# Performance work log

Hardware: AMD Instinct MI355X
Metric: run time of the kernel (lower is better)

Reference implementation:

```python
import jax, jax.numpy as jnp
import numpy as np

N_NODES = 100000
N_EDGES = 3200000


def setup_inputs() -> dict:
    key = jax.random.key(0)
    ks = jax.random.split(key, 20)
    x = jax.random.normal(ks[0], (N_NODES, 3), dtype=jnp.float32)
    edge_index = jax.random.randint(ks[1], (2, N_EDGES), 0, N_NODES, dtype=jnp.int64)

    def w(k, shape, fan_in):
        return jax.random.normal(k, shape, dtype=jnp.float32) * (1.0 / np.sqrt(fan_in))

    return {
        "x": x, "edge_index": edge_index,
        # layer 1: in=3, out=16, heads=2
        "W1": w(ks[2], (3, 32), 3), "a_src1": w(ks[3], (2, 16), 16), "a_dst1": w(ks[4], (2, 16), 16), "b1": jnp.zeros((32,), jnp.float32),
        # layer 2: in=32, out=16, heads=2
        "W2": w(ks[5], (32, 32), 32), "a_src2": w(ks[6], (2, 16), 16), "a_dst2": w(ks[7], (2, 16), 16), "b2": jnp.zeros((32,), jnp.float32),
        # layer 3: in=32, out=16, heads=1
        "W3": w(ks[8], (32, 16), 32), "a_src3": w(ks[9], (1, 16), 16), "a_dst3": w(ks[10], (1, 16), 16), "b3": jnp.zeros((16,), jnp.float32),
        # output linear 16 -> 1
        "Wout": w(ks[11], (16, 1), 16), "bout": jnp.zeros((1,), jnp.float32),
    }


def gat_layer(x, src, dst, W, a_src, a_dst, b, heads, ch, n):
    # h: [N, H, C]
    h = (x @ W).reshape(n, heads, ch)
    alpha_src = jnp.sum(h * a_src[None], axis=-1)  # [N, H]
    alpha_dst = jnp.sum(h * a_dst[None], axis=-1)  # [N, H]
    e = jax.nn.leaky_relu(alpha_src[src] + alpha_dst[dst], 0.2)  # [E, H]
    # segment softmax over incoming edges of each dst node
    m = jax.ops.segment_max(e, dst, num_segments=n)
    m = jnp.where(jnp.isfinite(m), m, 0.0)
    ex = jnp.exp(e - jax.lax.stop_gradient(m)[dst])
    s = jax.ops.segment_sum(ex, dst, num_segments=n)
    alpha = ex / (s[dst] + 1e-16)  # [E, H]
    out = jax.ops.segment_sum(h[src] * alpha[:, :, None], dst, num_segments=n)  # [N, H, C]
    return out.reshape(n, heads * ch) + b


def reference(x, edge_index, W1, a_src1, a_dst1, b1, W2, a_src2, a_dst2, b2,
              W3, a_src3, a_dst3, b3, Wout, bout):
    n = x.shape[0]
    loops = jnp.arange(n, dtype=edge_index.dtype)
    src = jnp.concatenate([edge_index[0], loops])  # PyG add_self_loops=True
    dst = jnp.concatenate([edge_index[1], loops])
    h = jax.nn.elu(gat_layer(x, src, dst, W1, a_src1, a_dst1, b1, 2, 16, n))
    h = jax.nn.elu(gat_layer(h, src, dst, W2, a_src2, a_dst2, b2, 2, 16, n))
    h = jax.nn.elu(gat_layer(h, src, dst, W3, a_src3, a_dst3, b3, 1, 16, n))
    embeddings = h
    out = jax.nn.sigmoid(h @ Wout + bout)
    return out, embeddings
```

## Files before the change

kernel.cpp:

```cpp
#include <hip/hip_runtime.h>
#include <math.h>

#define TPB 256
#define PMAX 128
#define PSH 10
#define PW  1024
#define CHUNK 8192

__device__ __forceinline__ float leaky02(float x) { return x > 0.f ? x : 0.2f * x; }
__device__ __forceinline__ float eluf(float x) { return x > 0.f ? x : (expf(x) - 1.f); }


__global__ void zero_kernel(int* __restrict__ p, int n) {
  int i = blockIdx.x * blockDim.x + threadIdx.x;
  if (i < n) p[i] = 0;
}

__global__ __launch_bounds__(256) void count_kernel(const int* __restrict__ dst, int E, int n,
                                                    int* __restrict__ counts,
                                                    int* __restrict__ pcount) {
  __shared__ int lcnt[PMAX];
  int Etot = E + n;
  int c0 = blockIdx.x * CHUNK;
  if (c0 >= Etot) return;
  int c1 = min(c0 + CHUNK, Etot);
  for (int j = threadIdx.x; j < PMAX; j += TPB) lcnt[j] = 0;
  __syncthreads();
  for (int idx = c0 + threadIdx.x; idx < c1; idx += TPB) {
    int dd = (idx < E) ? dst[idx] : (idx - E);
    atomicAdd(&lcnt[dd >> PSH], 1);
  }
  __syncthreads();
  for (int j = threadIdx.x; j < PMAX; j += TPB) {
    int v = lcnt[j];
    counts[blockIdx.x * PMAX + j] = v;
    if (v) atomicAdd(&pcount[j], v);
  }
}

__global__ void pscan_kernel(const int* __restrict__ pcount, int* __restrict__ pbase,
                             int* __restrict__ pcursor, int NP) {
  if (threadIdx.x == 0) {
    int acc = 0;
    for (int q = 0; q < NP; q++) {
      pbase[q] = acc; pcursor[q] = acc; acc += pcount[q];
    }
    pbase[NP] = acc;
  }
}

__global__ __launch_bounds__(256) void scatter_kernel(const int* __restrict__ src,
                                                      const int* __restrict__ dst,
                                                      int E, int n,
                                                      const int* __restrict__ counts,
                                                      int* __restrict__ pcursor,
                                                      unsigned* __restrict__ pstage) {
  __shared__ int lbase[PMAX];
  __shared__ int lcnt[PMAX];
  int Etot = E + n;
  int c0 = blockIdx.x * CHUNK;
  if (c0 >= Etot) return;
  int c1 = min(c0 + CHUNK, Etot);
  for (int j = threadIdx.x; j < PMAX; j += TPB) {
    int c = counts[blockIdx.x * PMAX + j];
    lbase[j] = atomicAdd(&pcursor[j], c);
    lcnt[j] = 0;
  }
  __syncthreads();
  for (int idx = c0 + threadIdx.x; idx < c1; idx += TPB) {
    int ss, dd;
    if (idx < E) { ss = src[idx]; dd = dst[idx]; }
    else         { ss = dd = idx - E; }
    int p = dd >> PSH;
    int pos = lbase[p] + atomicAdd(&lcnt[p], 1);
    pstage[pos] = ((unsigned)ss << PSH) | (unsigned)(dd & (PW - 1));
  }
}

__global__ __launch_bounds__(1024) void build_csr_kernel(const unsigned* __restrict__ pstage,
                                                         const int* __restrict__ pbase,
                                                         int nvtx,
                                                         int* __restrict__ rowptr,
                                                         int* __restrict__ csr_src) {
  __shared__ int lhist[PW];
  __shared__ int lcur[PW];
  int t = threadIdx.x;
  int p = blockIdx.x;
  int base = pbase[p];
  int end = pbase[p + 1];
  int nodebase = p << PSH;
  lhist[t] = 0;
  __syncthreads();
  for (int i = base + t; i < end; i += 1024)
    atomicAdd(&lhist[pstage[i] & (PW - 1)], 1);
  __syncthreads();
  int v = lhist[t];
  lcur[t] = v;
  __syncthreads();
  for (int off = 1; off < 1024; off <<= 1) {
    int a = (t >= off) ? lcur[t - off] : 0;
    __syncthreads();
    lcur[t] += a;
    __syncthreads();
  }
  int acc = base + lcur[t] - v;
  __syncthreads();
  lcur[t] = acc;
  int node = nodebase + t;
  if (node < nvtx) rowptr[node] = acc;
  __syncthreads();
  for (int i = base + t; i < end; i += 1024) {
    unsigned w = pstage[i];
    int pos = atomicAdd(&lcur[w & (PW - 1)], 1);
    csr_src[pos] = (int)(w >> PSH);
  }
  if (p == (int)gridDim.x - 1 && t == 0) rowptr[nvtx] = end;
}


template<int IN, int OUT, int H>
__global__ void transform_kernel(const float* __restrict__ x, const float* __restrict__ W,
                                 const float* __restrict__ a_src, const float* __restrict__ a_dst,
                                 float* __restrict__ h, float* __restrict__ asrc,
                                 float* __restrict__ adst, int n) {
  __shared__ float sW[IN * OUT];
  __shared__ float sa[2 * OUT];
  for (int i = threadIdx.x; i < IN * OUT; i += blockDim.x) sW[i] = W[i];
  if (threadIdx.x < OUT) {
    sa[threadIdx.x] = a_src[threadIdx.x];
    sa[OUT + threadIdx.x] = a_dst[threadIdx.x];
  }
  __syncthreads();
  int i = blockIdx.x * blockDim.x + threadIdx.x;
  if (i >= n) return;
  float xv[IN];
#pragma unroll
  for (int k = 0; k < IN; k++) xv[k] = x[(size_t)i * IN + k];
  float hv[OUT];
#pragma unroll
  for (int j = 0; j < OUT; j++) {
    float acc = 0.f;
#pragma unroll
    for (int k = 0; k < IN; k++) acc += xv[k] * sW[k * OUT + j];
    hv[j] = acc;
    h[(size_t)i * OUT + j] = acc;
  }
#pragma unroll
  for (int hh = 0; hh < H; hh++) {
    float as = 0.f, ad = 0.f;
#pragma unroll
    for (int c = 0; c < 16; c++) {
      as += hv[hh * 16 + c] * sa[hh * 16 + c];
      ad += hv[hh * 16 + c] * sa[OUT + hh * 16 + c];
    }
    asrc[i * H + hh] = as;
    adst[i * H + hh] = ad;
  }
}


__global__ __launch_bounds__(256) void node_gat12(
    const int* __restrict__ rowptr,
    const int* __restrict__ csr_src,
    const float* __restrict__ asrc,
    const float* __restrict__ adst,
    const float* __restrict__ hfeat,
    const float* __restrict__ bias,
    float* __restrict__ outb,
    int n) {
  __shared__ float2 s_h0[4][64];
  __shared__ float2 s_h1[4][64];
  int wid = threadIdx.x >> 6;
  int lane = threadIdx.x & 63;
  int i = (blockIdx.x * blockDim.x + threadIdx.x) >> 6;
  if (i >= n) return;
  int start = rowptr[i];
  int d = rowptr[i + 1] - start;
  float ad0 = adst[i * 2 + 0];
  float ad1 = adst[i * 2 + 1];
  const float4* hf4 = (const float4*)hfeat;
  int g = lane >> 3;
  int q = lane & 7;
  float4 acc = make_float4(0.f, 0.f, 0.f, 0.f);
  float sl0 = 0.f, sl1 = 0.f;

  if (d <= 64) {
    int sidx = 0;
    float e0 = -3.4e38f, e1 = -3.4e38f;
    if (lane < d) {
      sidx = csr_src[start + lane];
      float2 av = ((const float2*)asrc)[sidx];
      e0 = leaky02(av.x + ad0);
      e1 = leaky02(av.y + ad1);
    }
    float m0 = e0, m1 = e1;
#pragma unroll
    for (int off = 32; off >= 1; off >>= 1) {
      m0 = fmaxf(m0, __shfl_xor(m0, off));
      m1 = fmaxf(m1, __shfl_xor(m1, off));
    }
    float w0 = 0.f, w1 = 0.f;
    if (lane < d) { w0 = expf(e0 - m0); w1 = expf(e1 - m1); }
    sl0 = w0; sl1 = w1;
    s_h0[wid][lane] = make_float2(__int_as_float(sidx), w0);
    s_h1[wid][lane] = make_float2(__int_as_float(sidx), w1);
    for (int jj = g; jj < d; jj += 8) {
      float2 pw = (q >= 4) ? s_h1[wid][jj] : s_h0[wid][jj];
      int sb = __float_as_int(pw.x);
      float w = pw.y;
      float4 hv = hf4[(size_t)sb * 8 + q];
      acc.x += w * hv.x; acc.y += w * hv.y; acc.z += w * hv.z; acc.w += w * hv.w;
    }
  } else {
    float m0 = -3.4e38f, m1 = -3.4e38f;
    for (int k = lane; k < d; k += 64) {
      int sidx = csr_src[start + k];
      float2 av = ((const float2*)asrc)[sidx];
      m0 = fmaxf(m0, leaky02(av.x + ad0));
      m1 = fmaxf(m1, leaky02(av.y + ad1));
    }
#pragma unroll
    for (int off = 32; off >= 1; off >>= 1) {
      m0 = fmaxf(m0, __shfl_xor(m0, off));
      m1 = fmaxf(m1, __shfl_xor(m1, off));
    }
    for (int base = 0; base < d; base += 64) {
      int k = base + lane;
      int sidx = 0;
      float w0 = 0.f, w1 = 0.f;
      if (k < d) {
        sidx = csr_src[start + k];
        float2 av = ((const float2*)asrc)[sidx];
        w0 = expf(leaky02(av.x + ad0) - m0);
        w1 = expf(leaky02(av.y + ad1) - m1);
        sl0 += w0; sl1 += w1;
      }
      s_h0[wid][lane] = make_float2(__int_as_float(sidx), w0);
      s_h1[wid][lane] = make_float2(__int_as_float(sidx), w1);
      int cnt = min(64, d - base);
      for (int jj = g; jj < cnt; jj += 8) {
        float2 pw = (q >= 4) ? s_h1[wid][jj] : s_h0[wid][jj];
        int sb = __float_as_int(pw.x);
        float w = pw.y;
        float4 hv = hf4[(size_t)sb * 8 + q];
        acc.x += w * hv.x; acc.y += w * hv.y; acc.z += w * hv.z; acc.w += w * hv.w;
      }
    }
  }

#pragma unroll
  for (int off = 32; off >= 1; off >>= 1) {
    sl0 += __shfl_xor(sl0, off);
    sl1 += __shfl_xor(sl1, off);
  }
#pragma unroll
  for (int off = 8; off <= 32; off <<= 1) {
    acc.x += __shfl_xor(acc.x, off);
    acc.y += __shfl_xor(acc.y, off);
    acc.z += __shfl_xor(acc.z, off);
    acc.w += __shfl_xor(acc.w, off);
  }
  if (lane < 8) {
    float inv = 1.f / (((lane >= 4) ? sl1 : sl0) + 1e-16f);
    float4 bv = ((const float4*)bias)[lane];
    float4 o;
    o.x = eluf(acc.x * inv + bv.x);
    o.y = eluf(acc.y * inv + bv.y);
    o.z = eluf(acc.z * inv + bv.z);
    o.w = eluf(acc.w * inv + bv.w);
    ((float4*)outb)[(size_t)i * 8 + lane] = o;
  }
}

__global__ __launch_bounds__(256) void node_gat3(
    const int* __restrict__ rowptr,
    const int* __restrict__ csr_src,
    const float* __restrict__ asrc,
    const float* __restrict__ adst,
    const float* __restrict__ hfeat,
    const float* __restrict__ b3,
    const float* __restrict__ Wout,
    const float* __restrict__ bout,
    float* __restrict__ out,
    int n) {
  __shared__ float2 s_hw[4][64];
  int wid = threadIdx.x >> 6;
  int lane = threadIdx.x & 63;
  int i = (blockIdx.x * blockDim.x + threadIdx.x) >> 6;
  if (i >= n) return;
  int start = rowptr[i];
  int d = rowptr[i + 1] - start;
  float ad0 = adst[i];
  const float4* hf4 = (const float4*)hfeat;
  int g = lane >> 2;
  int q = lane & 3;
  float4 acc = make_float4(0.f, 0.f, 0.f, 0.f);
  float sl = 0.f;

  if (d <= 64) {
    int sidx = 0;
    float e0 = -3.4e38f;
    if (lane < d) {
      sidx = csr_src[start + lane];
      e0 = leaky02(asrc[sidx] + ad0);
    }
    float m0 = e0;
#pragma unroll
    for (int off = 32; off >= 1; off >>= 1) m0 = fmaxf(m0, __shfl_xor(m0, off));
    float w0 = (lane < d) ? expf(e0 - m0) : 0.f;
    sl = w0;
    s_hw[wid][lane] = make_float2(__int_as_float(sidx), w0);
    for (int jj = g; jj < d; jj += 16) {
      float2 pw = s_hw[wid][jj];
      int sb = __float_as_int(pw.x);
      float w = pw.y;
      float4 hv = hf4[(size_t)sb * 4 + q];
      acc.x += w * hv.x; acc.y += w * hv.y; acc.z += w * hv.z; acc.w += w * hv.w;
    }
  } else {
    float m0 = -3.4e38f;
    for (int k = lane; k < d; k += 64) {
      int sidx = csr_src[start + k];
      m0 = fmaxf(m0, leaky02(asrc[sidx] + ad0));
    }
#pragma unroll
    for (int off = 32; off >= 1; off >>= 1) m0 = fmaxf(m0, __shfl_xor(m0, off));
    for (int base = 0; base < d; base += 64) {
      int k = base + lane;
      int sidx = 0;
      float w0 = 0.f;
      if (k < d) {
        sidx = csr_src[start + k];
        w0 = expf(leaky02(asrc[sidx] + ad0) - m0);
        sl += w0;
      }
      s_hw[wid][lane] = make_float2(__int_as_float(sidx), w0);
      int cnt = min(64, d - base);
      for (int jj = g; jj < cnt; jj += 16) {
        float2 pw = s_hw[wid][jj];
        int sb = __float_as_int(pw.x);
        float w = pw.y;
        float4 hv = hf4[(size_t)sb * 4 + q];
        acc.x += w * hv.x; acc.y += w * hv.y; acc.z += w * hv.z; acc.w += w * hv.w;
      }
    }
  }

#pragma unroll
  for (int off = 32; off >= 1; off >>= 1) sl += __shfl_xor(sl, off);
#pragma unroll
  for (int off = 4; off <= 32; off <<= 1) {
    acc.x += __shfl_xor(acc.x, off);
    acc.y += __shfl_xor(acc.y, off);
    acc.z += __shfl_xor(acc.z, off);
    acc.w += __shfl_xor(acc.w, off);
  }
  float z = 0.f;
  if (lane < 4) {
    float inv = 1.f / (sl + 1e-16f);
    float4 bv = ((const float4*)b3)[lane];
    float4 wv = ((const float4*)Wout)[lane];
    float4 o;
    o.x = eluf(acc.x * inv + bv.x);
    o.y = eluf(acc.y * inv + bv.y);
    o.z = eluf(acc.z * inv + bv.z);
    o.w = eluf(acc.w * inv + bv.w);
    ((float4*)(out + n))[(size_t)i * 4 + lane] = o;
    z = o.x * wv.x + o.y * wv.y + o.z * wv.z + o.w * wv.w;
  }
  z += __shfl_xor(z, 1);
  z += __shfl_xor(z, 2);
  if (lane == 0) out[i] = 1.f / (1.f + expf(-(z + bout[0])));
}


extern "C" void kernel_launch(void* const* d_in, const int* in_sizes, int n_in,
                              void* d_out, int out_size, void* d_ws, size_t ws_size,
                              hipStream_t stream) {
  const float* x    = (const float*)d_in[0];
  const int*   ei   = (const int*)d_in[1];
  const float* W1   = (const float*)d_in[2];
  const float* as1  = (const float*)d_in[3];
  const float* ad1  = (const float*)d_in[4];
  const float* b1   = (const float*)d_in[5];
  const float* W2   = (const float*)d_in[6];
  const float* as2  = (const float*)d_in[7];
  const float* ad2  = (const float*)d_in[8];
  const float* b2   = (const float*)d_in[9];
  const float* W3   = (const float*)d_in[10];
  const float* as3  = (const float*)d_in[11];
  const float* ad3  = (const float*)d_in[12];
  const float* b3   = (const float*)d_in[13];
  const float* Wout = (const float*)d_in[14];
  const float* bout = (const float*)d_in[15];
  float* out = (float*)d_out;

  const int n = in_sizes[0] / 3;
  const int E = in_sizes[1] / 2;
  const int Etot = E + n;
  const int* src = ei;
  const int* dst = ei + E;
  const int NP = ((n - 1) >> PSH) + 1;
  const int nbC = (Etot + CHUNK - 1) / CHUNK;

  float* ws = (float*)d_ws;
  float* bufH = ws;
  float* bufX = bufH + (size_t)n * 32;
  float* asrc = bufX + (size_t)n * 32;
  float* adst = asrc + (size_t)n * 2;
  int* rowptr  = (int*)(adst + (size_t)n * 2);
  int* pbase   = rowptr + n + 1;
  int* pcursor = pbase + PMAX + 1;
  int* pcount  = pcursor + PMAX;
  int* csr_src = pcount + PMAX;
  int* counts  = csr_src + Etot;
  unsigned* pstage = (unsigned*)ws;

  const int nbN = (n + TPB - 1) / TPB;
  const int nbW = (n + 3) / 4;

  zero_kernel<<<1, PMAX, 0, stream>>>(pcount, PMAX);
  count_kernel<<<nbC, TPB, 0, stream>>>(dst, E, n, counts, pcount);
  pscan_kernel<<<1, 64, 0, stream>>>(pcount, pbase, pcursor, NP);
  scatter_kernel<<<nbC, TPB, 0, stream>>>(src, dst, E, n, counts, pcursor, pstage);
  build_csr_kernel<<<NP, 1024, 0, stream>>>(pstage, pbase, n, rowptr, csr_src);

  transform_kernel<3, 32, 2><<<nbN, TPB, 0, stream>>>(x, W1, as1, ad1, bufH, asrc, adst, n);
  node_gat12<<<nbW, TPB, 0, stream>>>(rowptr, csr_src, asrc, adst, bufH, b1, bufX, n);

  transform_kernel<32, 32, 2><<<nbN, TPB, 0, stream>>>(bufX, W2, as2, ad2, bufH, asrc, adst, n);
  node_gat12<<<nbW, TPB, 0, stream>>>(rowptr, csr_src, asrc, adst, bufH, b2, bufX, n);

  transform_kernel<32, 16, 1><<<nbN, TPB, 0, stream>>>(bufX, W3, as3, ad3, bufH, asrc, adst, n);
  node_gat3<<<nbW, TPB, 0, stream>>>(rowptr, csr_src, asrc, adst, bufH, b3, Wout, bout, out, n);
}
```

Measured before the change: 424.0 us.

## Drop zero kernel, parallelize partition scan, use fast exp and premultiplied indices

Removes the zeroing kernel and the global atomics on partition counts. The single-thread partition prefix sum is replaced by a 512-thread reduction over the per-block counts followed by a shared-memory scan. The 1024-wide scan in CSR building now uses wavefront shuffles instead of ten barrier rounds. The GAT aggregation kernels switch to __expf, store pre-shifted source indices, and pack both heads' weights into one float4 shared entry to drop the per-lane select and the 64-bit index math. Together these cut launch count, serial work and address arithmetic, at the cost of slightly lower exp precision.

```diff
diff --git a/kernel.cpp b/kernel.cpp
--- a/kernel.cpp
+++ b/kernel.cpp
@@ -8,17 +8,11 @@
 #define CHUNK 8192
 
 __device__ __forceinline__ float leaky02(float x) { return x > 0.f ? x : 0.2f * x; }
-__device__ __forceinline__ float eluf(float x) { return x > 0.f ? x : (expf(x) - 1.f); }
-
-
-__global__ void zero_kernel(int* __restrict__ p, int n) {
-  int i = blockIdx.x * blockDim.x + threadIdx.x;
-  if (i < n) p[i] = 0;
-}
+__device__ __forceinline__ float eluf(float x) { return x > 0.f ? x : (__expf(x) - 1.f); }
+
 
 __global__ __launch_bounds__(256) void count_kernel(const int* __restrict__ dst, int E, int n,
-                                                    int* __restrict__ counts,
-                                                    int* __restrict__ pcount) {
+                                                    int* __restrict__ counts) {
   __shared__ int lcnt[PMAX];
   int Etot = E + n;
   int c0 = blockIdx.x * CHUNK;
@@ -31,21 +25,42 @@
     atomicAdd(&lcnt[dd >> PSH], 1);
   }
   __syncthreads();
-  for (int j = threadIdx.x; j < PMAX; j += TPB) {
-    int v = lcnt[j];
-    counts[blockIdx.x * PMAX + j] = v;
-    if (v) atomicAdd(&pcount[j], v);
-  }
-}
-
-__global__ void pscan_kernel(const int* __restrict__ pcount, int* __restrict__ pbase,
-                             int* __restrict__ pcursor, int NP) {
-  if (threadIdx.x == 0) {
-    int acc = 0;
-    for (int q = 0; q < NP; q++) {
-      pbase[q] = acc; pcursor[q] = acc; acc += pcount[q];
-    }
-    pbase[NP] = acc;
+  for (int j = threadIdx.x; j < PMAX; j += TPB)
+    counts[blockIdx.x * PMAX + j] = lcnt[j];
+}
+
+__global__ __launch_bounds__(512) void pscan_kernel(const int* __restrict__ counts, int nbC,
+                                                    int* __restrict__ pbase,
+                                                    int* __restrict__ pcursor) {
+  __shared__ int part[4][PMAX];
+  __shared__ int ssum[PMAX];
+  int t = threadIdx.x;
+  int p = t & (PMAX - 1);
+  int sub = t >> 7;
+  int acc = 0;
+#pragma unroll 4
+  for (int b = sub; b < nbC; b += 4) acc += counts[b * PMAX + p];
+  part[sub][p] = acc;
+  __syncthreads();
+  int own = 0;
+  if (t < PMAX) {
+    own = part[0][t] + part[1][t] + part[2][t] + part[3][t];
+    ssum[t] = own;
+  }
+  __syncthreads();
+  for (int off = 1; off < PMAX; off <<= 1) {
+    int a = 0;
+    if (t < PMAX && t >= off) a = ssum[t - off];
+    __syncthreads();
+    if (t < PMAX) ssum[t] += a;
+    __syncthreads();
+  }
+  if (t < PMAX) {
+    int incl = ssum[t];
+    int excl = incl - own;
+    pbase[t] = excl;
+    pcursor[t] = excl;
+    if (t == PMAX - 1) pbase[PMAX] = incl;
   }
 }
 
@@ -85,6 +100,8 @@
   __shared__ int lhist[PW];
   __shared__ int lcur[PW];
   int t = threadIdx.x;
+  int lane = t & 63;
+  int wid = t >> 6;
   int p = blockIdx.x;
   int base = pbase[p];
   int end = pbase[p + 1];
@@ -95,15 +112,26 @@
     atomicAdd(&lhist[pstage[i] & (PW - 1)], 1);
   __syncthreads();
   int v = lhist[t];
-  lcur[t] = v;
-  __syncthreads();
-  for (int off = 1; off < 1024; off <<= 1) {
-    int a = (t >= off) ? lcur[t - off] : 0;
-    __syncthreads();
-    lcur[t] += a;
-    __syncthreads();
-  }
-  int acc = base + lcur[t] - v;
+  int x = v;
+#pragma unroll
+  for (int off = 1; off < 64; off <<= 1) {
+    int u = __shfl_up(x, off);
+    if (lane >= off) x += u;
+  }
+  if (lane == 63) lcur[wid] = x;
+  __syncthreads();
+  if (t < 16) {
+    int wsum = lcur[t];
+    int y = wsum;
+#pragma unroll
+    for (int off = 1; off < 16; off <<= 1) {
+      int u = __shfl_up(y, off);
+      if (t >= off) y += u;
+    }
+    lcur[t] = y - wsum;
+  }
+  __syncthreads();
+  int acc = base + x + lcur[wid] - v;
   __syncthreads();
   lcur[t] = acc;
   int node = nodebase + t;
@@ -168,8 +196,7 @@
     const float* __restrict__ bias,
     float* __restrict__ outb,
     int n) {
-  __shared__ float2 s_h0[4][64];
-  __shared__ float2 s_h1[4][64];
+  __shared__ float4 s_e[4][64];
   int wid = threadIdx.x >> 6;
   int lane = threadIdx.x & 63;
   int i = (blockIdx.x * blockDim.x + threadIdx.x) >> 6;
@@ -181,14 +208,16 @@
   const float4* hf4 = (const float4*)hfeat;
   int g = lane >> 3;
   int q = lane & 7;
+  const float2* sp = (const float2*)(&s_e[wid][0]) + (q >> 2);
   float4 acc = make_float4(0.f, 0.f, 0.f, 0.f);
   float sl0 = 0.f, sl1 = 0.f;
 
   if (d <= 64) {
-    int sidx = 0;
+    int sidx8 = 0;
     float e0 = -3.4e38f, e1 = -3.4e38f;
     if (lane < d) {
-      sidx = csr_src[start + lane];
+      int sidx = csr_src[start + lane];
+      sidx8 = sidx << 3;
       float2 av = ((const float2*)asrc)[sidx];
       e0 = leaky02(av.x + ad0);
       e1 = leaky02(av.y + ad1);
@@ -200,15 +229,14 @@
       m1 = fmaxf(m1, __shfl_xor(m1, off));
     }
     float w0 = 0.f, w1 = 0.f;
-    if (lane < d) { w0 = expf(e0 - m0); w1 = expf(e1 - m1); }
+    if (lane < d) { w0 = __expf(e0 - m0); w1 = __expf(e1 - m1); }
     sl0 = w0; sl1 = w1;
-    s_h0[wid][lane] = make_float2(__int_as_float(sidx), w0);
-    s_h1[wid][lane] = make_float2(__int_as_float(sidx), w1);
+    s_e[wid][lane] = make_float4(__int_as_float(sidx8), w0, __int_as_float(sidx8), w1);
     for (int jj = g; jj < d; jj += 8) {
-      float2 pw = (q >= 4) ? s_h1[wid][jj] : s_h0[wid][jj];
-      int sb = __float_as_int(pw.x);
+      float2 pw = sp[2 * jj];
+      int sb8 = __float_as_int(pw.x);
       float w = pw.y;
-      float4 hv = hf4[(size_t)sb * 8 + q];
+      float4 hv = hf4[sb8 + q];
       acc.x += w * hv.x; acc.y += w * hv.y; acc.z += w * hv.z; acc.w += w * hv.w;
     }
   } else {
@@ -226,23 +254,23 @@
     }
     for (int base = 0; base < d; base += 64) {
       int k = base + lane;
-      int sidx = 0;
+      int sidx8 = 0;
       float w0 = 0.f, w1 = 0.f;
       if (k < d) {
-        sidx = csr_src[start + k];
+        int sidx = csr_src[start + k];
+        sidx8 = sidx << 3;
         float2 av = ((const float2*)asrc)[sidx];
-        w0 = expf(leaky02(av.x + ad0) - m0);
-        w1 = expf(leaky02(av.y + ad1) - m1);
+        w0 = __expf(leaky02(av.x + ad0) - m0);
+        w1 = __expf(leaky02(av.y + ad1) - m1);
         sl0 += w0; sl1 += w1;
       }
-      s_h0[wid][lane] = make_float2(__int_as_float(sidx), w0);
-      s_h1[wid][lane] = make_float2(__int_as_float(sidx), w1);
+      s_e[wid][lane] = make_float4(__int_as_float(sidx8), w0, __int_as_float(sidx8), w1);
       int cnt = min(64, d - base);
       for (int jj = g; jj < cnt; jj += 8) {
-        float2 pw = (q >= 4) ? s_h1[wid][jj] : s_h0[wid][jj];
-        int sb = __float_as_int(pw.x);
+        float2 pw = sp[2 * jj];
+        int sb8 = __float_as_int(pw.x);
         float w = pw.y;
-        float4 hv = hf4[(size_t)sb * 8 + q];
+        float4 hv = hf4[sb8 + q];
         acc.x += w * hv.x; acc.y += w * hv.y; acc.z += w * hv.z; acc.w += w * hv.w;
       }
     }
@@ -294,27 +322,29 @@
   const float4* hf4 = (const float4*)hfeat;
   int g = lane >> 2;
   int q = lane & 3;
+  const float2* sp = s_hw[wid];
   float4 acc = make_float4(0.f, 0.f, 0.f, 0.f);
   float sl = 0.f;
 
   if (d <= 64) {
-    int sidx = 0;
+    int sidx4 = 0;
     float e0 = -3.4e38f;
     if (lane < d) {
-      sidx = csr_src[start + lane];
+      int sidx = csr_src[start + lane];
+      sidx4 = sidx << 2;
       e0 = leaky02(asrc[sidx] + ad0);
     }
     float m0 = e0;
 #pragma unroll
     for (int off = 32; off >= 1; off >>= 1) m0 = fmaxf(m0, __shfl_xor(m0, off));
-    float w0 = (lane < d) ? expf(e0 - m0) : 0.f;
+    float w0 = (lane < d) ? __expf(e0 - m0) : 0.f;
     sl = w0;
-    s_hw[wid][lane] = make_float2(__int_as_float(sidx), w0);
+    s_hw[wid][lane] = make_float2(__int_as_float(sidx4), w0);
     for (int jj = g; jj < d; jj += 16) {
-      float2 pw = s_hw[wid][jj];
-      int sb = __float_as_int(pw.x);
+      float2 pw = sp[jj];
+      int sb4 = __float_as_int(pw.x);
       float w = pw.y;
-      float4 hv = hf4[(size_t)sb * 4 + q];
+      float4 hv = hf4[sb4 + q];
       acc.x += w * hv.x; acc.y += w * hv.y; acc.z += w * hv.z; acc.w += w * hv.w;
     }
   } else {
@@ -327,20 +357,21 @@
     for (int off = 32; off >= 1; off >>= 1) m0 = fmaxf(m0, __shfl_xor(m0, off));
     for (int base = 0; base < d; base += 64) {
       int k = base + lane;
-      int sidx = 0;
+      int sidx4 = 0;
       float w0 = 0.f;
       if (k < d) {
-        sidx = csr_src[start + k];
-        w0 = expf(leaky02(asrc[sidx] + ad0) - m0);
+        int sidx = csr_src[start + k];
+        sidx4 = sidx << 2;
+        w0 = __expf(leaky02(asrc[sidx] + ad0) - m0);
         sl += w0;
       }
-      s_hw[wid][lane] = make_float2(__int_as_float(sidx), w0);
+      s_hw[wid][lane] = make_float2(__int_as_float(sidx4), w0);
       int cnt = min(64, d - base);
       for (int jj = g; jj < cnt; jj += 16) {
-        float2 pw = s_hw[wid][jj];
-        int sb = __float_as_int(pw.x);
+        float2 pw = sp[jj];
+        int sb4 = __float_as_int(pw.x);
         float w = pw.y;
-        float4 hv = hf4[(size_t)sb * 4 + q];
+        float4 hv = hf4[sb4 + q];
         acc.x += w * hv.x; acc.y += w * hv.y; acc.z += w * hv.z; acc.w += w * hv.w;
       }
     }
@@ -370,7 +401,7 @@
   }
   z += __shfl_xor(z, 1);
   z += __shfl_xor(z, 2);
-  if (lane == 0) out[i] = 1.f / (1.f + expf(-(z + bout[0])));
+  if (lane == 0) out[i] = 1.f / (1.f + __expf(-(z + bout[0])));
 }
 
 
@@ -400,8 +431,8 @@
   const int Etot = E + n;
   const int* src = ei;
   const int* dst = ei + E;
+  const int nbC = (Etot + CHUNK - 1) / CHUNK;
   const int NP = ((n - 1) >> PSH) + 1;
-  const int nbC = (Etot + CHUNK - 1) / CHUNK;
 
   float* ws = (float*)d_ws;
   float* bufH = ws;
@@ -419,9 +450,8 @@
   const int nbN = (n + TPB - 1) / TPB;
   const int nbW = (n + 3) / 4;
 
-  zero_kernel<<<1, PMAX, 0, stream>>>(pcount, PMAX);
-  count_kernel<<<nbC, TPB, 0, stream>>>(dst, E, n, counts, pcount);
-  pscan_kernel<<<1, 64, 0, stream>>>(pcount, pbase, pcursor, NP);
+  count_kernel<<<nbC, TPB, 0, stream>>>(dst, E, n, counts);
+  pscan_kernel<<<1, 512, 0, stream>>>(counts, nbC, pbase, pcursor);
   scatter_kernel<<<nbC, TPB, 0, stream>>>(src, dst, E, n, counts, pcursor, pstage);
   build_csr_kernel<<<NP, 1024, 0, stream>>>(pstage, pbase, n, rowptr, csr_src);
 
```

Result: faster. 411.0 us (-3.1%).
